# Performance work log

Measured on AMD Instinct MI355X. Metric: run time of the kernel, lower is better.

The kernel has to match this reference:

```python
import jax, jax.numpy as jnp
import numpy as np

M1, N1, M2, N2 = 32, 64, 24, 48  # Kronecker block dims; 32*24=768, 64*48=3072


def setup_inputs() -> dict:
    key = jax.random.key(0)
    k1, k2, k3, k4, k5 = jax.random.split(key, 5)
    rank = 64
    x = jax.random.normal(k1, (4, 4096, 768), dtype=jnp.float32)
    A_factors = jax.random.normal(k2, (M1 * N1, rank), dtype=jnp.float32) * 0.05
    B_factors = jax.random.normal(k3, (rank, M2 * N2), dtype=jnp.float32) * 0.05
    # 'Sparse' residual is materialized dense in the original module (to_dense()).
    Sparse = jax.random.normal(k4, (768, 3072), dtype=jnp.float32) * 0.02
    bias = jax.random.normal(k5, (3072,), dtype=jnp.float32) * 0.02
    return {"x": x, "A_factors": A_factors, "B_factors": B_factors,
            "Sparse": Sparse, "bias": bias}


def reference(x, A_factors, B_factors, Sparse, bias):
    # Low-rank product: [2048, r] @ [r, 1152] -> [2048, 1152]
    W_tilde = A_factors @ B_factors
    # Kronecker permute: (m1, n1, m2, n2) -> (m1, m2, n1, n2) -> [768, 3072]
    W_low = W_tilde.reshape(M1, N1, M2, N2).transpose(0, 2, 1, 3).reshape(
        M1 * M2, N1 * N2)
    W = W_low + Sparse
    # Dense GEMM: [B, S, 768] @ [768, 3072] + bias
    return x @ W + bias
```

## Files before the change

kernel.cpp:

```cpp
#include <hip/hip_runtime.h>
#include <hip/hip_bf16.h>
#include <stdint.h>

#define M_TOT 16384
#define N_TOT 3072
#define K_TOT 768

#define BM 256
#define BN 256
#define BK 32
#define NT (K_TOT / BK)

typedef __attribute__((ext_vector_type(8))) short short8;
typedef __attribute__((ext_vector_type(4))) float f32x4;

__device__ __forceinline__ unsigned short f2bf(float f) {
    union { float f; unsigned u; } v;
    v.f = f;
    unsigned r = v.u + 0x7FFFu + ((v.u >> 16) & 1u);
    return (unsigned short)(r >> 16);
}

__global__ __launch_bounds__(384) void prep_cvt_kernel(
    const float* __restrict__ Af, const float* __restrict__ Bf,
    const float* __restrict__ Sp, const float* __restrict__ x,
    unsigned short* __restrict__ xb, unsigned short* __restrict__ Wt) {
    __shared__ float a_sh[4][64];
    __shared__ float wrow[4][1160];
    const int tid = threadIdx.x;
    const int b = blockIdx.x;

    if (b < 512) {
        const int m1 = b >> 4;
        const int n10 = (b & 15) * 4;
        if (tid < 256) {
            int rr = tid >> 6, k = tid & 63;
            a_sh[rr][k] = Af[(size_t)(m1 * 64 + n10 + rr) * 64 + k];
        }
        __syncthreads();
        float acc[4][3] = {};
        #pragma unroll 2
        for (int k = 0; k < 64; ++k) {
            const float* brow = Bf + (size_t)k * 1152;
            float b0 = brow[tid], b1 = brow[tid + 384], b2 = brow[tid + 768];
            #pragma unroll
            for (int rr = 0; rr < 4; ++rr) {
                float a = a_sh[rr][k];
                acc[rr][0] = fmaf(a, b0, acc[rr][0]);
                acc[rr][1] = fmaf(a, b1, acc[rr][1]);
                acc[rr][2] = fmaf(a, b2, acc[rr][2]);
            }
        }
        #pragma unroll
        for (int rr = 0; rr < 4; ++rr) {
            wrow[rr][tid] = acc[rr][0];
            wrow[rr][tid + 384] = acc[rr][1];
            wrow[rr][tid + 768] = acc[rr][2];
        }
        __syncthreads();
        if (tid < 192) {
            const int rr = tid / 48, n2 = tid % 48;
            const int c = (n10 + rr) * 48 + n2;
            const int r0 = m1 * 24;
            unsigned w[12];
            #pragma unroll
            for (int t2 = 0; t2 < 12; ++t2) {
                float lo = wrow[rr][(2 * t2) * 48 + n2]
                         + Sp[(size_t)(r0 + 2 * t2) * 3072 + c];
                float hi = wrow[rr][(2 * t2 + 1) * 48 + n2]
                         + Sp[(size_t)(r0 + 2 * t2 + 1) * 3072 + c];
                w[t2] = (unsigned)f2bf(lo) | ((unsigned)f2bf(hi) << 16);
            }
            uint4* d4 = reinterpret_cast<uint4*>(Wt + (size_t)c * 768 + r0);
            d4[0] = (uint4){w[0], w[1], w[2], w[3]};
            d4[1] = (uint4){w[4], w[5], w[6], w[7]};
            d4[2] = (uint4){w[8], w[9], w[10], w[11]};
        }
    } else {
        const int n8 = M_TOT * K_TOT / 8;
        int i = (b - 512) * 384 + tid;
        const int stride = 2048 * 384;
        const float4* xv = reinterpret_cast<const float4*>(x);
        uint4* ov = reinterpret_cast<uint4*>(xb);
        for (; i < n8; i += stride) {
            float4 a = xv[2 * i], c = xv[2 * i + 1];
            uint4 o;
            o.x = (unsigned)f2bf(a.x) | ((unsigned)f2bf(a.y) << 16);
            o.y = (unsigned)f2bf(a.z) | ((unsigned)f2bf(a.w) << 16);
            o.z = (unsigned)f2bf(c.x) | ((unsigned)f2bf(c.y) << 16);
            o.w = (unsigned)f2bf(c.z) | ((unsigned)f2bf(c.w) << 16);
            ov[i] = o;
        }
    }
}

__device__ __forceinline__ void gld16(const void* g, void* l) {
    __builtin_amdgcn_global_load_lds(
        (const __attribute__((address_space(1))) void*)g,
        (__attribute__((address_space(3))) void*)l, 16, 0, 0);
}

__global__ __launch_bounds__(512, 2) void gemm_bt_kernel(
    const unsigned short* __restrict__ A, const unsigned short* __restrict__ Bt,
    const float* __restrict__ bias, float* __restrict__ C) {
    __shared__ unsigned short As[4][BM * BK];
    __shared__ unsigned short Bs[4][BN * BK];

    const int tid = threadIdx.x;
    const int lane = tid & 63;
    const int wid = tid >> 6;
    const int wr = wid >> 2;
    const int wc = wid & 3;

    const int wg = (blockIdx.x & 7) * 96 + (blockIdx.x >> 3);
    const int bm = wg / (N_TOT / BN), bn = wg % (N_TOT / BN);
    const int brow = bm * BM, bcol = bn * BN;

    const int srow = tid >> 2;
    const int soff = (((tid & 3) ^ ((tid >> 3) & 3)) << 4);
    const char* pA = (const char*)A + ((size_t)(brow + srow) * K_TOT) * 2 + soff;
    const char* pB = (const char*)Bt + ((size_t)(bcol + srow) * K_TOT) * 2 + soff;
    const size_t row128 = (size_t)128 * K_TOT * 2;
    const int tid16 = tid * 16;

#define STAGE_AH(u) do { const char* s_ = pA + (size_t)(u) * (BK * 2);           \
        gld16(s_,          (char*)&As[(u) & 3][0] + tid16);                      \
        gld16(s_ + row128, (char*)&As[(u) & 3][0] + tid16 + 8192); } while (0)
#define STAGE_BH(u) do { const char* s_ = pB + (size_t)(u) * (BK * 2);           \
        gld16(s_,          (char*)&Bs[(u) & 3][0] + tid16);                      \
        gld16(s_ + row128, (char*)&Bs[(u) & 3][0] + tid16 + 8192); } while (0)

    const int la = lane & 15;
    const int g4 = lane >> 4;
    const int swb = ((g4 ^ ((lane >> 1) & 3)) << 4);
#define FRAG_A(bu, r) (*(const short8*)((const char*)&As[bu][0] + (r) * 64 + swb))
#define FRAG_B(bu, r) (*(const short8*)((const char*)&Bs[bu][0] + (r) * 64 + swb))

    f32x4 acc[8][4];
    #pragma unroll
    for (int m = 0; m < 8; ++m)
        #pragma unroll
        for (int n = 0; n < 4; ++n)
            acc[m][n] = (f32x4){0.f, 0.f, 0.f, 0.f};

    const int arow = wr * 128;
    const int bcolw = wc * 64;

    short8 bE[4], bO[4], aLo[4], aHi[4];

    STAGE_AH(0); STAGE_BH(0);
    STAGE_AH(1); STAGE_BH(1);
    STAGE_AH(2); STAGE_BH(2);
    asm volatile("s_waitcnt vmcnt(4)" ::: "memory");
    __builtin_amdgcn_s_barrier();
    #pragma unroll
    for (int n = 0; n < 4; ++n) bE[n] = FRAG_B(0, bcolw + n * 16 + la);
    #pragma unroll
    for (int m = 0; m < 4; ++m) aLo[m] = FRAG_A(0, arow + m * 16 + la);
    __builtin_amdgcn_sched_barrier(0);

    auto tile_body = [&](int t, short8 (&bc)[4], short8 (&bnx)[4]) {
        const int bu = t & 3;
        #pragma unroll
        for (int m = 0; m < 4; ++m) aHi[m] = FRAG_A(bu, arow + 64 + m * 16 + la);
        if (t < NT - 3) STAGE_AH(t + 3);
        __builtin_amdgcn_sched_barrier(0);
        __builtin_amdgcn_s_barrier();
        __builtin_amdgcn_s_setprio(1);
        #pragma unroll
        for (int m = 0; m < 4; ++m)
            #pragma unroll
            for (int n = 0; n < 4; ++n)
                acc[m][n] = __builtin_amdgcn_mfma_f32_16x16x32_bf16(
                    bc[n], aLo[m], acc[m][n], 0, 0, 0);
        __builtin_amdgcn_s_setprio(0);
        __builtin_amdgcn_s_barrier();
        if (t < NT - 1) {
            const int bu1 = (t + 1) & 3;
            #pragma unroll
            for (int n = 0; n < 4; ++n) bnx[n] = FRAG_B(bu1, bcolw + n * 16 + la);
            #pragma unroll
            for (int m = 0; m < 4; ++m) aLo[m] = FRAG_A(bu1, arow + m * 16 + la);
        }
        if (t < NT - 3) STAGE_BH(t + 3);
        __builtin_amdgcn_sched_barrier(0);
        if (t < NT - 3)       asm volatile("s_waitcnt vmcnt(4)" ::: "memory");
        else if (t == NT - 3) asm volatile("s_waitcnt vmcnt(0)" ::: "memory");
        __builtin_amdgcn_s_barrier();
        __builtin_amdgcn_s_setprio(1);
        #pragma unroll
        for (int m = 0; m < 4; ++m)
            #pragma unroll
            for (int n = 0; n < 4; ++n)
                acc[4 + m][n] = __builtin_amdgcn_mfma_f32_16x16x32_bf16(
                    bc[n], aHi[m], acc[4 + m][n], 0, 0, 0);
        __builtin_amdgcn_s_setprio(0);
        __builtin_amdgcn_s_barrier();
    };

    #pragma unroll 1
    for (int tt = 0; tt < NT; tt += 2) {
        tile_body(tt, bE, bO);
        tile_body(tt + 1, bO, bE);
    }

    #pragma unroll
    for (int n = 0; n < 4; ++n) {
        const int gc = bcol + bcolw + n * 16 + g4 * 4;
        const f32x4 bv = *reinterpret_cast<const f32x4*>(&bias[gc]);
        #pragma unroll
        for (int m = 0; m < 8; ++m) {
            const int gr = brow + arow + m * 16 + la;
            f32x4 o = {acc[m][n][0] + bv[0], acc[m][n][1] + bv[1],
                       acc[m][n][2] + bv[2], acc[m][n][3] + bv[3]};
            *reinterpret_cast<f32x4*>(&C[(size_t)gr * N_TOT + gc]) = o;
        }
    }
#undef STAGE_AH
#undef STAGE_BH
#undef FRAG_A
#undef FRAG_B
}

extern "C" void kernel_launch(void* const* d_in, const int* in_sizes, int n_in,
                              void* d_out, int out_size, void* d_ws, size_t ws_size,
                              hipStream_t stream) {
    const float* x    = (const float*)d_in[0];
    const float* Af   = (const float*)d_in[1];
    const float* Bf   = (const float*)d_in[2];
    const float* Sp   = (const float*)d_in[3];
    const float* bias = (const float*)d_in[4];
    float* out = (float*)d_out;

    unsigned short* xb = (unsigned short*)d_ws;
    unsigned short* wt = xb + (size_t)M_TOT * K_TOT;

    hipLaunchKernelGGL(prep_cvt_kernel, dim3(512 + 2048), dim3(384), 0, stream,
                       Af, Bf, Sp, x, xb, wt);
    hipLaunchKernelGGL(gemm_bt_kernel,
                       dim3((M_TOT / BM) * (N_TOT / BN)), dim3(512),
                       0, stream, xb, wt, bias, out);
}
```

Baseline: 126.7 us.

## Load B fragments directly from global into registers, bypassing LDS

Removes the shared-memory staging buffers for the B operand. Each wave now loads its B MFMA fragments straight from global memory into registers, prefetched two K-tiles ahead. The per-tile schedule is simplified to a single wait-and-barrier, with A fragments read from LDS just before each half of the MFMA work. This cuts LDS traffic, LDS footprint and barrier count. In exchange, waves sharing columns issue redundant global loads for B, and register-level prefetch has to hide global/L2 latency.

```diff
diff --git a/kernel.cpp b/kernel.cpp
--- a/kernel.cpp
+++ b/kernel.cpp
@@ -104,7 +104,6 @@
     const unsigned short* __restrict__ A, const unsigned short* __restrict__ Bt,
     const float* __restrict__ bias, float* __restrict__ C) {
     __shared__ unsigned short As[4][BM * BK];
-    __shared__ unsigned short Bs[4][BN * BK];
 
     const int tid = threadIdx.x;
     const int lane = tid & 63;
@@ -119,22 +118,24 @@
     const int srow = tid >> 2;
     const int soff = (((tid & 3) ^ ((tid >> 3) & 3)) << 4);
     const char* pA = (const char*)A + ((size_t)(brow + srow) * K_TOT) * 2 + soff;
-    const char* pB = (const char*)Bt + ((size_t)(bcol + srow) * K_TOT) * 2 + soff;
     const size_t row128 = (size_t)128 * K_TOT * 2;
     const int tid16 = tid * 16;
 
 #define STAGE_AH(u) do { const char* s_ = pA + (size_t)(u) * (BK * 2);           \
         gld16(s_,          (char*)&As[(u) & 3][0] + tid16);                      \
         gld16(s_ + row128, (char*)&As[(u) & 3][0] + tid16 + 8192); } while (0)
-#define STAGE_BH(u) do { const char* s_ = pB + (size_t)(u) * (BK * 2);           \
-        gld16(s_,          (char*)&Bs[(u) & 3][0] + tid16);                      \
-        gld16(s_ + row128, (char*)&Bs[(u) & 3][0] + tid16 + 8192); } while (0)
 
     const int la = lane & 15;
     const int g4 = lane >> 4;
     const int swb = ((g4 ^ ((lane >> 1) & 3)) << 4);
 #define FRAG_A(bu, r) (*(const short8*)((const char*)&As[bu][0] + (r) * 64 + swb))
-#define FRAG_B(bu, r) (*(const short8*)((const char*)&Bs[bu][0] + (r) * 64 + swb))
+
+    const int bcolw = wc * 64;
+    const short8* pBn[4];
+    #pragma unroll
+    for (int n = 0; n < 4; ++n)
+        pBn[n] = reinterpret_cast<const short8*>(
+            Bt + (size_t)(bcol + bcolw + n * 16 + la) * K_TOT + g4 * 8);
 
     f32x4 acc[8][4];
     #pragma unroll
@@ -143,65 +144,59 @@
         for (int n = 0; n < 4; ++n)
             acc[m][n] = (f32x4){0.f, 0.f, 0.f, 0.f};
 
-    const int arow = wr * 128;
-    const int bcolw = wc * 64;
-
-    short8 bE[4], bO[4], aLo[4], aHi[4];
-
-    STAGE_AH(0); STAGE_BH(0);
-    STAGE_AH(1); STAGE_BH(1);
-    STAGE_AH(2); STAGE_BH(2);
+    short8 bEv[4], bOd[4];
+    #pragma unroll
+    for (int n = 0; n < 4; ++n) bEv[n] = pBn[n][0];
+    #pragma unroll
+    for (int n = 0; n < 4; ++n) bOd[n] = pBn[n][4];
+    STAGE_AH(0); STAGE_AH(1); STAGE_AH(2);
     asm volatile("s_waitcnt vmcnt(4)" ::: "memory");
     __builtin_amdgcn_s_barrier();
-    #pragma unroll
-    for (int n = 0; n < 4; ++n) bE[n] = FRAG_B(0, bcolw + n * 16 + la);
-    #pragma unroll
-    for (int m = 0; m < 4; ++m) aLo[m] = FRAG_A(0, arow + m * 16 + la);
     __builtin_amdgcn_sched_barrier(0);
 
-    auto tile_body = [&](int t, short8 (&bc)[4], short8 (&bnx)[4]) {
+    const int arow = wr * 128;
+
+    auto body = [&](int t, short8 (&bc)[4]) {
         const int bu = t & 3;
-        #pragma unroll
-        for (int m = 0; m < 4; ++m) aHi[m] = FRAG_A(bu, arow + 64 + m * 16 + la);
+        short8 a_[4];
+        #pragma unroll
+        for (int m = 0; m < 4; ++m) a_[m] = FRAG_A(bu, arow + m * 16 + la);
         if (t < NT - 3) STAGE_AH(t + 3);
-        __builtin_amdgcn_sched_barrier(0);
-        __builtin_amdgcn_s_barrier();
         __builtin_amdgcn_s_setprio(1);
         #pragma unroll
         for (int m = 0; m < 4; ++m)
             #pragma unroll
             for (int n = 0; n < 4; ++n)
                 acc[m][n] = __builtin_amdgcn_mfma_f32_16x16x32_bf16(
-                    bc[n], aLo[m], acc[m][n], 0, 0, 0);
+                    bc[n], a_[m], acc[m][n], 0, 0, 0);
         __builtin_amdgcn_s_setprio(0);
-        __builtin_amdgcn_s_barrier();
-        if (t < NT - 1) {
-            const int bu1 = (t + 1) & 3;
-            #pragma unroll
-            for (int n = 0; n < 4; ++n) bnx[n] = FRAG_B(bu1, bcolw + n * 16 + la);
-            #pragma unroll
-            for (int m = 0; m < 4; ++m) aLo[m] = FRAG_A(bu1, arow + m * 16 + la);
-        }
-        if (t < NT - 3) STAGE_BH(t + 3);
-        __builtin_amdgcn_sched_barrier(0);
-        if (t < NT - 3)       asm volatile("s_waitcnt vmcnt(4)" ::: "memory");
-        else if (t == NT - 3) asm volatile("s_waitcnt vmcnt(0)" ::: "memory");
-        __builtin_amdgcn_s_barrier();
+        #pragma unroll
+        for (int m = 0; m < 4; ++m) a_[m] = FRAG_A(bu, arow + 64 + m * 16 + la);
         __builtin_amdgcn_s_setprio(1);
         #pragma unroll
         for (int m = 0; m < 4; ++m)
             #pragma unroll
             for (int n = 0; n < 4; ++n)
                 acc[4 + m][n] = __builtin_amdgcn_mfma_f32_16x16x32_bf16(
-                    bc[n], aHi[m], acc[4 + m][n], 0, 0, 0);
+                    bc[n], a_[m], acc[4 + m][n], 0, 0, 0);
         __builtin_amdgcn_s_setprio(0);
-        __builtin_amdgcn_s_barrier();
+        if (t + 2 < NT) {
+            #pragma unroll
+            for (int n = 0; n < 4; ++n) bc[n] = pBn[n][(t + 2) * 4];
+        }
+        if (t < NT - 1) {
+            if (t < NT - 3)       asm volatile("s_waitcnt vmcnt(6)" ::: "memory");
+            else if (t == NT - 3) asm volatile("s_waitcnt vmcnt(4)" ::: "memory");
+            else                  asm volatile("s_waitcnt vmcnt(0)" ::: "memory");
+            __builtin_amdgcn_s_barrier();
+            __builtin_amdgcn_sched_barrier(0);
+        }
     };
 
     #pragma unroll 1
     for (int tt = 0; tt < NT; tt += 2) {
-        tile_body(tt, bE, bO);
-        tile_body(tt + 1, bO, bE);
+        body(tt, bEv);
+        body(tt + 1, bOd);
     }
 
     #pragma unroll
@@ -217,9 +212,7 @@
         }
     }
 #undef STAGE_AH
-#undef STAGE_BH
 #undef FRAG_A
-#undef FRAG_B
 }
 
 extern "C" void kernel_launch(void* const* d_in, const int* in_sizes, int n_in,
```

Result: slower. 153.2 us (+20.9%).
